# Kernel optimization log

Hardware: AMD Instinct MI355X
Metric: run time of the kernel (lower is better)

The kernel has to match this reference:

```python
import jax, jax.numpy as jnp
import numpy as np
from jax import lax

H_PARAM = 1.0
SEARCH_WINDOW = 11  # r = 5 -> 121 shifts
PATCH = 5           # 5x5 box sum, circular boundary (torch.roll semantics)


def _box_sum_circular(t, p):
    # t: (B,1,H,W). Circular (wrap) boundary to match torch.roll-based BoxFilter.
    r = p // 2
    padded = jnp.pad(t, ((0, 0), (0, 0), (r, r), (r, r)), mode='wrap')
    kernel = jnp.ones((1, 1, p, p), dtype=t.dtype)
    return lax.conv_general_dilated(
        padded, kernel, window_strides=(1, 1), padding='VALID',
        dimension_numbers=('NCHW', 'OIHW', 'NCHW'))


def setup_inputs() -> dict:
    key = jax.random.key(0)
    rgb = jax.random.uniform(key, (8, 3, 1024, 1024), dtype=jnp.float32)
    return {"rgb": rgb}


def reference(rgb) -> jnp.ndarray:
    r = SEARCH_WINDOW // 2
    inv_h = 1.0 / (H_PARAM + 1e-6)
    y = jnp.mean(rgb, axis=1, keepdims=True)  # (B,1,H,W) luminance

    # all (y_shift, x_shift) offsets in the search window, scanned sequentially
    offs = np.stack(np.meshgrid(np.arange(-r, r + 1), np.arange(-r, r + 1),
                                indexing='ij'), axis=-1).reshape(-1, 2)
    offs = jnp.asarray(offs, dtype=jnp.int32)  # (121, 2) -> (y_shift, x_shift)

    def step(carry, shift):
        denoised, weights = carry
        dy, dx = shift[0], shift[1]
        shifted_rgb = jnp.roll(rgb, (dy, dx), axis=(2, 3))
        shifted_y = jnp.roll(y, (dy, dx), axis=(2, 3))
        dist = jnp.sqrt(_box_sum_circular((y - shifted_y) ** 2, PATCH))
        w = lax.stop_gradient(jnp.exp(-dist * inv_h))  # torch.no_grad block
        return (denoised + shifted_rgb * w, weights + w), None

    init = (jnp.zeros_like(rgb), jnp.zeros_like(y))
    (denoised, weights), _ = lax.scan(step, init, offs)
    return denoised / weights
```

## Files before the change

### kernel.cpp

```cpp
#include <hip/hip_runtime.h>


#define HW (1024 * 1024)
#define W 1024
#define MASK 1023

constexpr int TILE = 32;
constexpr int YREG = 46;
constexpr int YPITCH = 48;
constexpr int CREG = 42;
constexpr float K3 = 1.4426935981939074f / 3.0f;

#define SBAR() __builtin_amdgcn_sched_barrier(0)

#define CR5(W0,W1,W2,W3,W4) \
    fmaf(c4,(W4), fmaf(c3,(W3), fmaf(c2,(W2), fmaf(c1,(W1), c0*(W0)))))

#define ROW_HA(RR)                                                          \
    const float* ycp = &ldsY[yci + (RR) * YPITCH];                          \
    const float* ywp = &ldsY[ywi + (RR) * YPITCH];                          \
    const float c0=ycp[0],c1=ycp[1],c2=ycp[2],c3=ycp[3],c4=ycp[4];          \
    const float w5 =ywp[5], w6 =ywp[6], w7 =ywp[7], w8 =ywp[8], w9 =ywp[9]; \
    const float w10=ywp[10],w11=ywp[11],w12=ywp[12],w13=ywp[13],w14=ywp[14];\
    const float h0 = CR5(w10,w11,w12,w13,w14);                              \
    const float h1 = CR5(w9, w10,w11,w12,w13);                              \
    const float h2 = CR5(w8, w9, w10,w11,w12);                              \
    const float h3 = CR5(w7, w8, w9, w10,w11);                              \
    const float h4 = CR5(w6, w7, w8, w9, w10);                              \
    const float h5 = CR5(w5, w6, w7, w8, w9);

#define ROW_HB(RR)                                                          \
    const float* ycp = &ldsY[yci + (RR) * YPITCH];                          \
    const float* ywp = &ldsY[ywi + (RR) * YPITCH];                          \
    const float c0=ycp[0],c1=ycp[1],c2=ycp[2],c3=ycp[3],c4=ycp[4];          \
    const float w0 =ywp[0], w1 =ywp[1], w2 =ywp[2], w3 =ywp[3], w4 =ywp[4]; \
    const float w5 =ywp[5], w6 =ywp[6], w7 =ywp[7], w8 =ywp[8];             \
    const float h6  = CR5(w4, w5, w6, w7, w8);                              \
    const float h7  = CR5(w3, w4, w5, w6, w7);                              \
    const float h8  = CR5(w2, w3, w4, w5, w6);                              \
    const float h9  = CR5(w1, w2, w3, w4, w5);                              \
    const float h10 = CR5(w0, w1, w2, w3, w4);

#define VDECLA(VD) float VD##_0, VD##_1, VD##_2, VD##_3, VD##_4, VD##_5
#define VSETA(VD)  VD##_0 =h0; VD##_1 =h1; VD##_2 =h2;                      \
                   VD##_3 =h3; VD##_4 =h4; VD##_5 =h5
#define VADDA(VD)  VD##_0+=h0; VD##_1+=h1; VD##_2+=h2;                      \
                   VD##_3+=h3; VD##_4+=h4; VD##_5+=h5
#define VDECLB(VD) float VD##_6, VD##_7, VD##_8, VD##_9, VD##_10
#define VSETB(VD)  VD##_6 =h6; VD##_7 =h7; VD##_8 =h8;                      \
                   VD##_9 =h9; VD##_10=h10
#define VADDB(VD)  VD##_6+=h6; VD##_7+=h7; VD##_8+=h8;                      \
                   VD##_9+=h9; VD##_10+=h10

#define FIN1(YO, VD, J) do {                                                \
    float4 px = crow[-(J)];                                                 \
    float s = fmaf(-2.0f, VD##_##J, acb + px.w);                            \
    float dist = __builtin_amdgcn_sqrtf(__builtin_fabsf(s));                \
    float wgt  = __builtin_amdgcn_exp2f(-dist);                             \
    aR##YO = fmaf(wgt, px.x, aR##YO);                                       \
    aG##YO = fmaf(wgt, px.y, aG##YO);                                       \
    aB##YO = fmaf(wgt, px.z, aB##YO);                                       \
    aW##YO += wgt;                                                          \
} while (0)

#define FIN_A(YO, VD) do {                                                  \
    const float4* crow = &ldsC[cri + (YO) * CREG];                          \
    const float acb = ldsC[abi + (YO) * CREG].w;                            \
    FIN1(YO,VD,0); FIN1(YO,VD,1); FIN1(YO,VD,2);                            \
    FIN1(YO,VD,3); FIN1(YO,VD,4); FIN1(YO,VD,5);                            \
} while (0)

#define FIN_B(YO, VD) do {                                                  \
    const float4* crow = &ldsC[cri + (YO) * CREG];                          \
    const float acb = ldsC[abi + (YO) * CREG].w;                            \
    FIN1(YO,VD,6); FIN1(YO,VD,7); FIN1(YO,VD,8);                            \
    FIN1(YO,VD,9); FIN1(YO,VD,10);                                          \
} while (0)

#define STORE(YO) do {                                                      \
    const int off = (by0 + y0 + (YO)) * W + bx0 + tx;                       \
    const float inv = 1.0f / aW##YO;                                        \
    obase[off]          = aR##YO * inv;                                     \
    obase[off + HW]     = aG##YO * inv;                                     \
    obase[off + 2 * HW] = aB##YO * inv;                                     \
} while (0)

#define A5(p) fmaf((p)[4],(p)[4], fmaf((p)[3],(p)[3], fmaf((p)[2],(p)[2],   \
              fmaf((p)[1],(p)[1], (p)[0]*(p)[0]))))

__global__ void __launch_bounds__(256) __attribute__((amdgpu_waves_per_eu(4, 4)))
nlm_fused(const float* __restrict__ rgb, float* __restrict__ out) {
    __shared__ float  ldsY[YREG * YPITCH];
    __shared__ float4 ldsC[CREG * CREG];

    const int tid = threadIdx.x;
    const int batch = blockIdx.z;
    const int by0 = blockIdx.y * TILE;
    const int bx0 = blockIdx.x * TILE;

    const float* base = rgb + (size_t)batch * 3 * HW;

    for (int i = tid; i < YREG * YREG; i += 256) {
        int ry = i / YREG, rx = i - ry * YREG;
        int gy = (by0 + ry - 7) & MASK;
        int gx = (bx0 + rx - 7) & MASK;
        int off = gy * W + gx;
        float v = (base[off] + base[off + HW] + base[off + 2 * HW]) * K3;
        ldsY[ry * YPITCH + rx] = v;
    }
    __syncthreads();

    for (int i = tid; i < CREG * CREG; i += 256) {
        int ry = i / CREG, rx = i - ry * CREG;
        int gy = (by0 + ry - 5) & MASK;
        int gx = (bx0 + rx - 5) & MASK;
        int off = gy * W + gx;
        const float* yb = &ldsY[ry * YPITCH + rx];
        float a =  A5(yb);
        a += A5(yb + YPITCH);
        a += A5(yb + 2 * YPITCH);
        a += A5(yb + 3 * YPITCH);
        a += A5(yb + 4 * YPITCH);
        ldsC[i] = make_float4(base[off], base[off + HW], base[off + 2 * HW], a);
    }
    __syncthreads();

    const int tx = tid & 31;
    const int y0 = (tid >> 5) * 4;

    const int yci = (y0 + 5) * YPITCH + tx + 5;
    const int abi = (y0 + 5) * CREG + tx + 5;

    float aR0=0.f, aG0=0.f, aB0=0.f, aW0=0.f;
    float aR1=0.f, aG1=0.f, aB1=0.f, aW1=0.f;
    float aR2=0.f, aG2=0.f, aB2=0.f, aW2=0.f;
    float aR3=0.f, aG3=0.f, aB3=0.f, aW3=0.f;

    #pragma clang loop unroll(disable)
    for (int dy = -5; dy <= 5; ++dy) {
        const int ywi = (y0 + 5 - dy) * YPITCH + tx;
        const int cri = (y0 - dy + 5) * CREG + tx + 10;
        {
            VDECLA(v0); VDECLA(v1); VDECLA(v2); VDECLA(v3);
            { ROW_HA(0); VSETA(v0); }                          SBAR();
            { ROW_HA(1); VADDA(v0); VSETA(v1); }               SBAR();
            { ROW_HA(2); VADDA(v0); VADDA(v1); VSETA(v2); }    SBAR();
            { ROW_HA(3); VADDA(v0); VADDA(v1); VADDA(v2); VSETA(v3); } SBAR();
            { ROW_HA(4); VADDA(v0); VADDA(v1); VADDA(v2); VADDA(v3); } SBAR();
            FIN_A(0, v0);                                      SBAR();
            { ROW_HA(5); VADDA(v1); VADDA(v2); VADDA(v3); }    SBAR();
            FIN_A(1, v1);                                      SBAR();
            { ROW_HA(6); VADDA(v2); VADDA(v3); }               SBAR();
            FIN_A(2, v2);                                      SBAR();
            { ROW_HA(7); VADDA(v3); }                          SBAR();
            FIN_A(3, v3);                                      SBAR();
        }
        {
            VDECLB(v0); VDECLB(v1); VDECLB(v2); VDECLB(v3);
            { ROW_HB(0); VSETB(v0); }                          SBAR();
            { ROW_HB(1); VADDB(v0); VSETB(v1); }               SBAR();
            { ROW_HB(2); VADDB(v0); VADDB(v1); VSETB(v2); }    SBAR();
            { ROW_HB(3); VADDB(v0); VADDB(v1); VADDB(v2); VSETB(v3); } SBAR();
            { ROW_HB(4); VADDB(v0); VADDB(v1); VADDB(v2); VADDB(v3); } SBAR();
            FIN_B(0, v0);                                      SBAR();
            { ROW_HB(5); VADDB(v1); VADDB(v2); VADDB(v3); }    SBAR();
            FIN_B(1, v1);                                      SBAR();
            { ROW_HB(6); VADDB(v2); VADDB(v3); }               SBAR();
            FIN_B(2, v2);                                      SBAR();
            { ROW_HB(7); VADDB(v3); }                          SBAR();
            FIN_B(3, v3);                                      SBAR();
        }
    }

    float* obase = out + (size_t)batch * 3 * HW;
    STORE(0);
    STORE(1);
    STORE(2);
    STORE(3);
}

extern "C" void kernel_launch(void* const* d_in, const int* in_sizes, int n_in,
                              void* d_out, int out_size, void* d_ws, size_t ws_size,
                              hipStream_t stream) {
    const float* rgb = (const float*)d_in[0];
    float* out = (float*)d_out;
    dim3 grid(W / TILE, W / TILE, 8);
    dim3 block(256, 1, 1);
    hipLaunchKernelGGL(nlm_fused, grid, block, 0, stream, rgb, out);
}
```

Baseline: 777.2 us.

## Read shifted RGB from global/L1 instead of staging float4 tile in LDS

The inner loop now loads the shifted RGB samples directly from global memory through the cache, and keeps only the per-pixel squared-luminance sums in LDS as a scalar array. This shrinks LDS use and per-sample LDS traffic. Interior tiles use plain offsets and edge tiles use masked wrap-around indexing. The waves_per_eu attribute is dropped, so the compiler chooses occupancy itself. The cost is many more global/L1 loads in the hot loop, with their extra latency and address arithmetic.

```diff
diff --git a/kernel.cpp b/kernel.cpp
--- a/kernel.cpp
+++ b/kernel.cpp
@@ -52,29 +52,53 @@
 #define VADDB(VD)  VD##_6+=h6; VD##_7+=h7; VD##_8+=h8;                      \
                    VD##_9+=h9; VD##_10+=h10
 
-#define FIN1(YO, VD, J) do {                                                \
-    float4 px = crow[-(J)];                                                 \
-    float s = fmaf(-2.0f, VD##_##J, acb + px.w);                            \
+#define FIN1G(YO, VD, J, IDXE) do {                                         \
+    const int gi = (IDXE);                                                  \
+    const float pr = gr[gi];                                                \
+    const float pg = gg[gi];                                                \
+    const float pb = gb[gi];                                                \
+    const float aw = ldsA[ari - (J)];                                       \
+    float s = fmaf(-2.0f, VD##_##J, acb + aw);                              \
     float dist = __builtin_amdgcn_sqrtf(__builtin_fabsf(s));                \
     float wgt  = __builtin_amdgcn_exp2f(-dist);                             \
-    aR##YO = fmaf(wgt, px.x, aR##YO);                                       \
-    aG##YO = fmaf(wgt, px.y, aG##YO);                                       \
-    aB##YO = fmaf(wgt, px.z, aB##YO);                                       \
+    aR##YO = fmaf(wgt, pr, aR##YO);                                         \
+    aG##YO = fmaf(wgt, pg, aG##YO);                                         \
+    aB##YO = fmaf(wgt, pb, aB##YO);                                         \
     aW##YO += wgt;                                                          \
 } while (0)
 
-#define FIN_A(YO, VD) do {                                                  \
-    const float4* crow = &ldsC[cri + (YO) * CREG];                          \
-    const float acb = ldsC[abi + (YO) * CREG].w;                            \
-    FIN1(YO,VD,0); FIN1(YO,VD,1); FIN1(YO,VD,2);                            \
-    FIN1(YO,VD,3); FIN1(YO,VD,4); FIN1(YO,VD,5);                            \
-} while (0)
-
-#define FIN_B(YO, VD) do {                                                  \
-    const float4* crow = &ldsC[cri + (YO) * CREG];                          \
-    const float acb = ldsC[abi + (YO) * CREG].w;                            \
-    FIN1(YO,VD,6); FIN1(YO,VD,7); FIN1(YO,VD,8);                            \
-    FIN1(YO,VD,9); FIN1(YO,VD,10);                                          \
+#define FIN_HEADG(YO)                                                       \
+    const int rowo = ((by0 + y0 + (YO) - dy) & MASK) << 10;                 \
+    const int ari  = cri + (YO) * CREG;                                     \
+    const float acb = ldsA[abi + (YO) * CREG];
+
+#define FIN_AF(YO, VD) do { FIN_HEADG(YO)                                   \
+    const int pre = rowo + txo;                                             \
+    FIN1G(YO,VD,0,pre  ); FIN1G(YO,VD,1,pre-1); FIN1G(YO,VD,2,pre-2);       \
+    SBAR();                                                                 \
+    FIN1G(YO,VD,3,pre-3); FIN1G(YO,VD,4,pre-4); FIN1G(YO,VD,5,pre-5);       \
+} while (0)
+
+#define FIN_BF(YO, VD) do { FIN_HEADG(YO)                                   \
+    const int pre = rowo + txo;                                             \
+    FIN1G(YO,VD,6,pre-6); FIN1G(YO,VD,7,pre-7); FIN1G(YO,VD,8,pre-8);       \
+    SBAR();                                                                 \
+    FIN1G(YO,VD,9,pre-9); FIN1G(YO,VD,10,pre-10);                           \
+} while (0)
+
+#define FIN_AE(YO, VD) do { FIN_HEADG(YO)                                   \
+    FIN1G(YO,VD,0,rowo+((txo  )&MASK)); FIN1G(YO,VD,1,rowo+((txo-1)&MASK)); \
+    FIN1G(YO,VD,2,rowo+((txo-2)&MASK));                                     \
+    SBAR();                                                                 \
+    FIN1G(YO,VD,3,rowo+((txo-3)&MASK)); FIN1G(YO,VD,4,rowo+((txo-4)&MASK)); \
+    FIN1G(YO,VD,5,rowo+((txo-5)&MASK));                                     \
+} while (0)
+
+#define FIN_BE(YO, VD) do { FIN_HEADG(YO)                                   \
+    FIN1G(YO,VD,6,rowo+((txo-6)&MASK)); FIN1G(YO,VD,7,rowo+((txo-7)&MASK)); \
+    FIN1G(YO,VD,8,rowo+((txo-8)&MASK));                                     \
+    SBAR();                                                                 \
+    FIN1G(YO,VD,9,rowo+((txo-9)&MASK)); FIN1G(YO,VD,10,rowo+((txo-10)&MASK));\
 } while (0)
 
 #define STORE(YO) do {                                                      \
@@ -88,40 +112,76 @@
 #define A5(p) fmaf((p)[4],(p)[4], fmaf((p)[3],(p)[3], fmaf((p)[2],(p)[2],   \
               fmaf((p)[1],(p)[1], (p)[0]*(p)[0]))))
 
-__global__ void __launch_bounds__(256) __attribute__((amdgpu_waves_per_eu(4, 4)))
+#define DY_BODY(FINAM, FINBM)                                               \
+    _Pragma("clang loop unroll(disable)")                                   \
+    for (int dy = -5; dy <= 5; ++dy) {                                      \
+        const int ywi = (y0 + 5 - dy) * YPITCH + tx;                        \
+        const int cri = (y0 - dy + 5) * CREG + tx + 10;                     \
+        {                                \
+            VDECLA(v0); VDECLA(v1); VDECLA(v2); VDECLA(v3);                 \
+            { ROW_HA(0); VSETA(v0); }                          SBAR();      \
+            { ROW_HA(1); VADDA(v0); VSETA(v1); }               SBAR();      \
+            { ROW_HA(2); VADDA(v0); VADDA(v1); VSETA(v2); }    SBAR();      \
+            { ROW_HA(3); VADDA(v0); VADDA(v1); VADDA(v2); VSETA(v3); } SBAR(); \
+            { ROW_HA(4); VADDA(v0); VADDA(v1); VADDA(v2); VADDA(v3); } SBAR(); \
+            FINAM(0, v0);                                      SBAR();      \
+            { ROW_HA(5); VADDA(v1); VADDA(v2); VADDA(v3); }    SBAR();      \
+            FINAM(1, v1);                                      SBAR();      \
+            { ROW_HA(6); VADDA(v2); VADDA(v3); }               SBAR();      \
+            FINAM(2, v2);                                      SBAR();      \
+            { ROW_HA(7); VADDA(v3); }                          SBAR();      \
+            FINAM(3, v3);                                      SBAR();      \
+        }                                                                   \
+        {                                \
+            VDECLB(v0); VDECLB(v1); VDECLB(v2); VDECLB(v3);                 \
+            { ROW_HB(0); VSETB(v0); }                          SBAR();      \
+            { ROW_HB(1); VADDB(v0); VSETB(v1); }               SBAR();      \
+            { ROW_HB(2); VADDB(v0); VADDB(v1); VSETB(v2); }    SBAR();      \
+            { ROW_HB(3); VADDB(v0); VADDB(v1); VADDB(v2); VSETB(v3); } SBAR(); \
+            { ROW_HB(4); VADDB(v0); VADDB(v1); VADDB(v2); VADDB(v3); } SBAR(); \
+            FINBM(0, v0);                                      SBAR();      \
+            { ROW_HB(5); VADDB(v1); VADDB(v2); VADDB(v3); }    SBAR();      \
+            FINBM(1, v1);                                      SBAR();      \
+            { ROW_HB(6); VADDB(v2); VADDB(v3); }               SBAR();      \
+            FINBM(2, v2);                                      SBAR();      \
+            { ROW_HB(7); VADDB(v3); }                          SBAR();      \
+            FINBM(3, v3);                                      SBAR();      \
+        }                                                                   \
+    }
+
+__global__ void __launch_bounds__(256)
 nlm_fused(const float* __restrict__ rgb, float* __restrict__ out) {
-    __shared__ float  ldsY[YREG * YPITCH];
-    __shared__ float4 ldsC[CREG * CREG];
+    __shared__ float ldsY[YREG * YPITCH];
+    __shared__ float ldsA[CREG * CREG];
 
     const int tid = threadIdx.x;
     const int batch = blockIdx.z;
     const int by0 = blockIdx.y * TILE;
     const int bx0 = blockIdx.x * TILE;
 
-    const float* base = rgb + (size_t)batch * 3 * HW;
+    const float* gr = rgb + (size_t)batch * 3 * HW;
+    const float* gg = gr + HW;
+    const float* gb = gr + 2 * HW;
 
     for (int i = tid; i < YREG * YREG; i += 256) {
         int ry = i / YREG, rx = i - ry * YREG;
         int gy = (by0 + ry - 7) & MASK;
         int gx = (bx0 + rx - 7) & MASK;
         int off = gy * W + gx;
-        float v = (base[off] + base[off + HW] + base[off + 2 * HW]) * K3;
+        float v = (gr[off] + gg[off] + gb[off]) * K3;
         ldsY[ry * YPITCH + rx] = v;
     }
     __syncthreads();
 
     for (int i = tid; i < CREG * CREG; i += 256) {
         int ry = i / CREG, rx = i - ry * CREG;
-        int gy = (by0 + ry - 5) & MASK;
-        int gx = (bx0 + rx - 5) & MASK;
-        int off = gy * W + gx;
         const float* yb = &ldsY[ry * YPITCH + rx];
         float a =  A5(yb);
         a += A5(yb + YPITCH);
         a += A5(yb + 2 * YPITCH);
         a += A5(yb + 3 * YPITCH);
         a += A5(yb + 4 * YPITCH);
-        ldsC[i] = make_float4(base[off], base[off + HW], base[off + 2 * HW], a);
+        ldsA[i] = a;
     }
     __syncthreads();
 
@@ -130,46 +190,17 @@
 
     const int yci = (y0 + 5) * YPITCH + tx + 5;
     const int abi = (y0 + 5) * CREG + tx + 5;
+    const int txo = bx0 + tx + 5;
 
     float aR0=0.f, aG0=0.f, aB0=0.f, aW0=0.f;
     float aR1=0.f, aG1=0.f, aB1=0.f, aW1=0.f;
     float aR2=0.f, aG2=0.f, aB2=0.f, aW2=0.f;
     float aR3=0.f, aG3=0.f, aB3=0.f, aW3=0.f;
 
-    #pragma clang loop unroll(disable)
-    for (int dy = -5; dy <= 5; ++dy) {
-        const int ywi = (y0 + 5 - dy) * YPITCH + tx;
-        const int cri = (y0 - dy + 5) * CREG + tx + 10;
-        {
-            VDECLA(v0); VDECLA(v1); VDECLA(v2); VDECLA(v3);
-            { ROW_HA(0); VSETA(v0); }                          SBAR();
-            { ROW_HA(1); VADDA(v0); VSETA(v1); }               SBAR();
-            { ROW_HA(2); VADDA(v0); VADDA(v1); VSETA(v2); }    SBAR();
-            { ROW_HA(3); VADDA(v0); VADDA(v1); VADDA(v2); VSETA(v3); } SBAR();
-            { ROW_HA(4); VADDA(v0); VADDA(v1); VADDA(v2); VADDA(v3); } SBAR();
-            FIN_A(0, v0);                                      SBAR();
-            { ROW_HA(5); VADDA(v1); VADDA(v2); VADDA(v3); }    SBAR();
-            FIN_A(1, v1);                                      SBAR();
-            { ROW_HA(6); VADDA(v2); VADDA(v3); }               SBAR();
-            FIN_A(2, v2);                                      SBAR();
-            { ROW_HA(7); VADDA(v3); }                          SBAR();
-            FIN_A(3, v3);                                      SBAR();
-        }
-        {
-            VDECLB(v0); VDECLB(v1); VDECLB(v2); VDECLB(v3);
-            { ROW_HB(0); VSETB(v0); }                          SBAR();
-            { ROW_HB(1); VADDB(v0); VSETB(v1); }               SBAR();
-            { ROW_HB(2); VADDB(v0); VADDB(v1); VSETB(v2); }    SBAR();
-            { ROW_HB(3); VADDB(v0); VADDB(v1); VADDB(v2); VSETB(v3); } SBAR();
-            { ROW_HB(4); VADDB(v0); VADDB(v1); VADDB(v2); VADDB(v3); } SBAR();
-            FIN_B(0, v0);                                      SBAR();
-            { ROW_HB(5); VADDB(v1); VADDB(v2); VADDB(v3); }    SBAR();
-            FIN_B(1, v1);                                      SBAR();
-            { ROW_HB(6); VADDB(v2); VADDB(v3); }               SBAR();
-            FIN_B(2, v2);                                      SBAR();
-            { ROW_HB(7); VADDB(v3); }                          SBAR();
-            FIN_B(3, v3);                                      SBAR();
-        }
+    if (bx0 >= 32 && bx0 <= 1024 - 64) {
+        DY_BODY(FIN_AF, FIN_BF);
+    } else {
+        DY_BODY(FIN_AE, FIN_BE);
     }
 
     float* obase = out + (size_t)batch * 3 * HW;
```

Result: slower. 1.019 ms (+31.2%).

## Use 512 threads per tile with two output rows per thread

Applied to the files above, without the earlier changes.

Doubles the block size to 512 threads and halves each thread's output rows from four to two, changing the sliding vertical box-sum pipeline to cover two rows. This puts more waves on each 32x32 tile and lowers register pressure per thread. In exchange, the vertical reuse of horizontal patch sums drops: each thread computes 6 horizontal rows for 2 outputs instead of 8 rows for 4, so more LDS reads and ALU work per output pixel.

```diff
diff --git a/kernel.cpp b/kernel.cpp
--- a/kernel.cpp
+++ b/kernel.cpp
@@ -88,7 +88,7 @@
 #define A5(p) fmaf((p)[4],(p)[4], fmaf((p)[3],(p)[3], fmaf((p)[2],(p)[2],   \
               fmaf((p)[1],(p)[1], (p)[0]*(p)[0]))))
 
-__global__ void __launch_bounds__(256) __attribute__((amdgpu_waves_per_eu(4, 4)))
+__global__ void __launch_bounds__(512) __attribute__((amdgpu_waves_per_eu(4, 4)))
 nlm_fused(const float* __restrict__ rgb, float* __restrict__ out) {
     __shared__ float  ldsY[YREG * YPITCH];
     __shared__ float4 ldsC[CREG * CREG];
@@ -100,7 +100,7 @@
 
     const float* base = rgb + (size_t)batch * 3 * HW;
 
-    for (int i = tid; i < YREG * YREG; i += 256) {
+    for (int i = tid; i < YREG * YREG; i += 512) {
         int ry = i / YREG, rx = i - ry * YREG;
         int gy = (by0 + ry - 7) & MASK;
         int gx = (bx0 + rx - 7) & MASK;
@@ -110,7 +110,7 @@
     }
     __syncthreads();
 
-    for (int i = tid; i < CREG * CREG; i += 256) {
+    for (int i = tid; i < CREG * CREG; i += 512) {
         int ry = i / CREG, rx = i - ry * CREG;
         int gy = (by0 + ry - 5) & MASK;
         int gx = (bx0 + rx - 5) & MASK;
@@ -126,57 +126,45 @@
     __syncthreads();
 
     const int tx = tid & 31;
-    const int y0 = (tid >> 5) * 4;
+    const int y0 = (tid >> 5) * 2;
 
     const int yci = (y0 + 5) * YPITCH + tx + 5;
     const int abi = (y0 + 5) * CREG + tx + 5;
 
     float aR0=0.f, aG0=0.f, aB0=0.f, aW0=0.f;
     float aR1=0.f, aG1=0.f, aB1=0.f, aW1=0.f;
-    float aR2=0.f, aG2=0.f, aB2=0.f, aW2=0.f;
-    float aR3=0.f, aG3=0.f, aB3=0.f, aW3=0.f;
 
     #pragma clang loop unroll(disable)
     for (int dy = -5; dy <= 5; ++dy) {
         const int ywi = (y0 + 5 - dy) * YPITCH + tx;
         const int cri = (y0 - dy + 5) * CREG + tx + 10;
         {
-            VDECLA(v0); VDECLA(v1); VDECLA(v2); VDECLA(v3);
-            { ROW_HA(0); VSETA(v0); }                          SBAR();
-            { ROW_HA(1); VADDA(v0); VSETA(v1); }               SBAR();
-            { ROW_HA(2); VADDA(v0); VADDA(v1); VSETA(v2); }    SBAR();
-            { ROW_HA(3); VADDA(v0); VADDA(v1); VADDA(v2); VSETA(v3); } SBAR();
-            { ROW_HA(4); VADDA(v0); VADDA(v1); VADDA(v2); VADDA(v3); } SBAR();
-            FIN_A(0, v0);                                      SBAR();
-            { ROW_HA(5); VADDA(v1); VADDA(v2); VADDA(v3); }    SBAR();
-            FIN_A(1, v1);                                      SBAR();
-            { ROW_HA(6); VADDA(v2); VADDA(v3); }               SBAR();
-            FIN_A(2, v2);                                      SBAR();
-            { ROW_HA(7); VADDA(v3); }                          SBAR();
-            FIN_A(3, v3);                                      SBAR();
+            VDECLA(v0); VDECLA(v1);
+            { ROW_HA(0); VSETA(v0); }               SBAR();
+            { ROW_HA(1); VADDA(v0); VSETA(v1); }    SBAR();
+            { ROW_HA(2); VADDA(v0); VADDA(v1); }    SBAR();
+            { ROW_HA(3); VADDA(v0); VADDA(v1); }    SBAR();
+            { ROW_HA(4); VADDA(v0); VADDA(v1); }    SBAR();
+            FIN_A(0, v0);                           SBAR();
+            { ROW_HA(5); VADDA(v1); }               SBAR();
+            FIN_A(1, v1);                           SBAR();
         }
         {
-            VDECLB(v0); VDECLB(v1); VDECLB(v2); VDECLB(v3);
-            { ROW_HB(0); VSETB(v0); }                          SBAR();
-            { ROW_HB(1); VADDB(v0); VSETB(v1); }               SBAR();
-            { ROW_HB(2); VADDB(v0); VADDB(v1); VSETB(v2); }    SBAR();
-            { ROW_HB(3); VADDB(v0); VADDB(v1); VADDB(v2); VSETB(v3); } SBAR();
-            { ROW_HB(4); VADDB(v0); VADDB(v1); VADDB(v2); VADDB(v3); } SBAR();
-            FIN_B(0, v0);                                      SBAR();
-            { ROW_HB(5); VADDB(v1); VADDB(v2); VADDB(v3); }    SBAR();
-            FIN_B(1, v1);                                      SBAR();
-            { ROW_HB(6); VADDB(v2); VADDB(v3); }               SBAR();
-            FIN_B(2, v2);                                      SBAR();
-            { ROW_HB(7); VADDB(v3); }                          SBAR();
-            FIN_B(3, v3);                                      SBAR();
+            VDECLB(v0); VDECLB(v1);
+            { ROW_HB(0); VSETB(v0); }               SBAR();
+            { ROW_HB(1); VADDB(v0); VSETB(v1); }    SBAR();
+            { ROW_HB(2); VADDB(v0); VADDB(v1); }    SBAR();
+            { ROW_HB(3); VADDB(v0); VADDB(v1); }    SBAR();
+            { ROW_HB(4); VADDB(v0); VADDB(v1); }    SBAR();
+            FIN_B(0, v0);                           SBAR();
+            { ROW_HB(5); VADDB(v1); }               SBAR();
+            FIN_B(1, v1);                           SBAR();
         }
     }
 
     float* obase = out + (size_t)batch * 3 * HW;
     STORE(0);
     STORE(1);
-    STORE(2);
-    STORE(3);
 }
 
 extern "C" void kernel_launch(void* const* d_in, const int* in_sizes, int n_in,
@@ -185,6 +173,6 @@
     const float* rgb = (const float*)d_in[0];
     float* out = (float*)d_out;
     dim3 grid(W / TILE, W / TILE, 8);
-    dim3 block(256, 1, 1);
+    dim3 block(512, 1, 1);
     hipLaunchKernelGGL(nlm_fused, grid, block, 0, stream, rgb, out);
 }
```

Result: slower. 876.0 us (+12.7%).
